# Kernel tuning notes

Hardware: AMD Instinct MI355X
Metric: run time of the kernel (lower is better)

## Reference

```python
import jax, jax.numpy as jnp
import numpy as np

B, L, D, H = 8, 512, 1024, 16
HD = D // H
DIST_VOCAB = 64
NEG = -1e9


def setup_inputs() -> dict:
    key = jax.random.key(0)
    ks = jax.random.split(key, 16)
    inp = {}
    inp['q'] = jax.random.normal(ks[0], (B, L, D), jnp.float32)
    inp['k'] = jax.random.normal(ks[1], (B, L, D), jnp.float32)
    inp['v'] = jax.random.normal(ks[2], (B, L, D), jnp.float32)
    s = 1.0 / np.sqrt(D)
    inp['Wq'] = jax.random.normal(ks[3], (D, D), jnp.float32) * s
    inp['bq'] = jnp.zeros((D,), jnp.float32)
    inp['Wk'] = jax.random.normal(ks[4], (D, D), jnp.float32) * s
    inp['bk'] = jnp.zeros((D,), jnp.float32)
    inp['Wv'] = jax.random.normal(ks[5], (D, D), jnp.float32) * s
    inp['bv'] = jnp.zeros((D,), jnp.float32)
    inp['Wo'] = jax.random.normal(ks[6], (D, D), jnp.float32) * s
    inp['bo'] = jnp.zeros((D,), jnp.float32)
    inp['dist_emb'] = jax.random.normal(ks[7], (DIST_VOCAB, H), jnp.float32) * (1.0 / np.sqrt(H))
    # sinusoidal positional table (1, L, D), rank-3 as asserted in AttentionBase
    pos = np.arange(L)[:, None]
    dim = np.arange(D)[None, :]
    ang = pos / np.power(10000.0, (2 * (dim // 2)) / D)
    pe = np.where(dim % 2 == 0, np.sin(ang), np.cos(ang)).astype(np.float32)
    inp['sin_enc'] = jnp.asarray(pe)[None]
    inp['length'] = jax.random.randint(ks[8], (B,), L // 2, L + 1, jnp.int32)
    inp['dist'] = jax.random.randint(ks[9], (B, L, L), 0, DIST_VOCAB, jnp.int32)
    return inp


def _rope(x, sin_pos, cos_pos):
    # x: (B, L, D). rotate-half interleaved: [-x1, x0, -x3, x2, ...]
    x_shift = jnp.stack([-x[..., 1::2], x[..., 0::2]], axis=-1).reshape(x.shape)
    return x * cos_pos + x_shift * sin_pos


def reference(q, k, v, Wq, bq, Wk, bk, Wv, bv, Wo, bo, dist_emb, sin_enc, length, dist):
    # linear projections (torch Linear: x @ W.T + b)
    qp = q @ Wq.T + bq
    kp = k @ Wk.T + bk
    vp = v @ Wv.T + bv
    # rope (pe='rope', cls_len=0, step=0)
    sin_pos = jnp.repeat(sin_enc[:, :L, 0::2], 2, axis=-1)
    cos_pos = jnp.repeat(sin_enc[:, :L, 1::2], 2, axis=-1)
    qp = _rope(qp, sin_pos, cos_pos)
    kp = _rope(kp, sin_pos, cos_pos)
    # split heads -> (B, H, L, HD)
    qh = qp.reshape(B, L, H, HD).transpose(0, 2, 1, 3)
    kh = kp.reshape(B, L, H, HD).transpose(0, 2, 1, 3)
    vh = vp.reshape(B, L, H, HD).transpose(0, 2, 1, 3)
    # scale (scale_length=0 -> 1/sqrt(d_head))
    qh = qh * (1.0 / np.sqrt(HD))
    scores = jnp.einsum('bhqd,bhkd->bhqk', qh, kh)
    # relative 'dist' bias: (B,L,L,H) -> (B,H,L,L)
    scores = scores + dist_emb[dist].transpose(0, 3, 1, 2)
    # padding mask: key positions >= valid length (future=False)
    key_mask = jnp.arange(L)[None, :] >= length[:, None]  # (B, L)
    scores = jnp.where(key_mask[:, None, None, :], NEG, scores)
    attn = jax.nn.softmax(scores, axis=-1)  # dropout p=0.0 => identity
    out = jnp.einsum('bhqk,bhkd->bhqd', attn, vh)
    out = out.transpose(0, 2, 1, 3).reshape(B, L, D)
    return out @ Wo.T + bo
```

## Files before the change

kernel.cpp:

```cpp
#include <hip/hip_runtime.h>
#include <stdint.h>

typedef unsigned short u16;
typedef __bf16 bf16x8 __attribute__((ext_vector_type(8)));
typedef float f32x4 __attribute__((ext_vector_type(4)));

#define MFMA16(a, b, c) __builtin_amdgcn_mfma_f32_16x16x32_bf16(a, b, c, 0, 0, 0)

__device__ __forceinline__ float b2f(u16 u) { return __uint_as_float(((uint32_t)u) << 16); }
__device__ __forceinline__ u16 f2b(float f) {
    uint32_t x = __float_as_uint(f);
    return (u16)((x + 0x7fffu + ((x >> 16) & 1u)) >> 16);
}
__device__ __forceinline__ void load16(const void* g, void* l) {
    __builtin_amdgcn_global_load_lds(
        (const __attribute__((address_space(1))) uint32_t*)(uintptr_t)g,
        (__attribute__((address_space(3))) uint32_t*)(uint32_t)(uintptr_t)l,
        16, 0, 0);
}
__device__ __forceinline__ bf16x8 ld8f(const float* f) {
    float4 a = *(const float4*)f;
    float4 b = *(const float4*)(f + 4);
    bf16x8 o;
    o[0] = (__bf16)a.x; o[1] = (__bf16)a.y; o[2] = (__bf16)a.z; o[3] = (__bf16)a.w;
    o[4] = (__bf16)b.x; o[5] = (__bf16)b.y; o[6] = (__bf16)b.z; o[7] = (__bf16)b.w;
    return o;
}

__global__ __launch_bounds__(256) void convert_k(
    const float* __restrict__ q, const float* __restrict__ k, const float* __restrict__ v,
    const float* __restrict__ Wq, const float* __restrict__ Wk,
    const float* __restrict__ Wv, const float* __restrict__ Wo,
    u16* __restrict__ qb, u16* __restrict__ kb, u16* __restrict__ vb,
    u16* __restrict__ wqb, u16* __restrict__ wkb, u16* __restrict__ wvb,
    u16* __restrict__ wob)
{
    const float* src; u16* dst; int n8;
    switch (blockIdx.y) {
        case 0: src = q;  dst = qb;  n8 = 524288; break;
        case 1: src = k;  dst = kb;  n8 = 524288; break;
        case 2: src = v;  dst = vb;  n8 = 524288; break;
        case 3: src = Wq; dst = wqb; n8 = 131072; break;
        case 4: src = Wk; dst = wkb; n8 = 131072; break;
        case 5: src = Wv; dst = wvb; n8 = 131072; break;
        default: src = Wo; dst = wob; n8 = 131072; break;
    }
    int i = blockIdx.x * 256 + threadIdx.x;
    if (i >= n8) return;
    bf16x8 o = ld8f(src + (size_t)i * 8);
    *(bf16x8*)(dst + (size_t)i * 8) = o;
}

__global__ __launch_bounds__(256) void gemm_proj_b(
    const u16* __restrict__ qb, const u16* __restrict__ kb, const u16* __restrict__ vb,
    const u16* __restrict__ wqb, const u16* __restrict__ wkb, const u16* __restrict__ wvb,
    const float* __restrict__ bq, const float* __restrict__ bk, const float* __restrict__ bv,
    const float* __restrict__ sin_enc,
    u16* __restrict__ qh, u16* __restrict__ kh, u16* __restrict__ vt)
{
    __shared__ __align__(16) u16 lA[128 * 32];
    __shared__ __align__(16) u16 lB[128 * 32];
    const int t = threadIdx.x, wave = t >> 6, lane = t & 63;
    const int bx = blockIdx.x;
    const int w_idx = bx >> 3;
    const int n0 = (bx & 7) << 7;
    const int m0 = blockIdx.y << 7;
    const u16* A = (w_idx == 0) ? qb : (w_idx == 1 ? kb : vb);
    const u16* W = (w_idx == 0) ? wqb : (w_idx == 1 ? wkb : wvb);
    const float* bias = (w_idx == 0) ? bq : (w_idx == 1 ? bk : bv);

    const int wr = wave >> 1, wc = wave & 1;
    const int col16 = lane & 15, g16 = lane >> 4;
    f32x4 acc[4][4] = {};

    const int r0  = wave * 32 + (lane >> 2);
    const int kc8 = (lane & 3) << 3;
    const u16* gA = A + (size_t)(m0 + r0) * 1024 + kc8;
    const u16* gB = W + (size_t)(n0 + r0) * 1024 + kc8;
    char* lA0 = (char*)lA + wave * 2048;
    char* lB0 = (char*)lB + wave * 2048;

    for (int kk = 0; kk < 1024; kk += 32) {
        load16(gA + kk, lA0);
        load16(gA + kk + 16 * 1024, lA0 + 1024);
        load16(gB + kk, lB0);
        load16(gB + kk + 16 * 1024, lB0 + 1024);
        __syncthreads();
        const u16* pA = lA + (wr * 64 + col16) * 32 + g16 * 8;
        const u16* pB = lB + (wc * 64 + col16) * 32 + g16 * 8;
        bf16x8 af[4], bfr[4];
#pragma unroll
        for (int i = 0; i < 4; i++) {
            af[i]  = *(const bf16x8*)(pA + i * 512);
            bfr[i] = *(const bf16x8*)(pB + i * 512);
        }
#pragma unroll
        for (int mi = 0; mi < 4; mi++)
#pragma unroll
            for (int ni = 0; ni < 4; ni++)
                acc[mi][ni] = MFMA16(af[mi], bfr[ni], acc[mi][ni]);
        __syncthreads();
    }

#pragma unroll
    for (int ni = 0; ni < 4; ni++) {
        const int n = n0 + wc * 64 + ni * 16 + col16;
        const float bn = bias[n];
        const int h = n >> 6, hd = n & 63;
#pragma unroll
        for (int mi = 0; mi < 4; mi++) {
#pragma unroll
            for (int r = 0; r < 4; r++) {
                const int m = m0 + wr * 64 + mi * 16 + g16 * 4 + r;
                const int b = m >> 9, l = m & 511;
                float x = acc[mi][ni][r] + bn;
                if (w_idx == 2) {
                    vt[((size_t)(b * 16 + h) * 64 + hd) * 512 + l] = f2b(x);
                } else {
                    float partner = __shfl_xor(x, 1);
                    float s = sin_enc[(size_t)l * 1024 + (n & ~1)];
                    float c = sin_enc[(size_t)l * 1024 + (n | 1)];
                    float y = (n & 1) ? (x * c + partner * s) : (x * c - partner * s);
                    if (w_idx == 0) y *= 0.125f;
                    u16* dst = (w_idx == 0) ? qh : kh;
                    dst[((size_t)(b * 16 + h) * 512 + l) * 64 + hd] = f2b(y);
                }
            }
        }
    }
}

__global__ __launch_bounds__(256) void gemm_proj_f32(
    const float* __restrict__ qin, const float* __restrict__ kin, const float* __restrict__ vin,
    const float* __restrict__ Wq, const float* __restrict__ bq,
    const float* __restrict__ Wk, const float* __restrict__ bk,
    const float* __restrict__ Wv, const float* __restrict__ bv,
    const float* __restrict__ sin_enc,
    u16* __restrict__ qh, u16* __restrict__ kh, u16* __restrict__ vt)
{
    __shared__ __align__(16) u16 lA[128 * 32];
    __shared__ __align__(16) u16 lB[128 * 32];
    const int t = threadIdx.x, wave = t >> 6, lane = t & 63;
    const int bx = blockIdx.x;
    const int w_idx = bx >> 3;
    const int n0 = (bx & 7) << 7;
    const int m0 = blockIdx.y << 7;
    const float* A    = (w_idx == 0) ? qin : (w_idx == 1 ? kin : vin);
    const float* W    = (w_idx == 0) ? Wq  : (w_idx == 1 ? Wk  : Wv);
    const float* bias = (w_idx == 0) ? bq  : (w_idx == 1 ? bk  : bv);

    const int wr = wave >> 1, wc = wave & 1;
    const int col16 = lane & 15, g16 = lane >> 4;
    f32x4 acc[4][4] = {};

    const int c0   = wave * 128 + lane;
    const int row0 = c0 >> 2;
    const int kp   = (c0 & 3) << 3;
    const size_t gA0 = (size_t)(m0 + row0) * 1024 + kp;
    const size_t gB0 = (size_t)(n0 + row0) * 1024 + kp;
    u16* wA0 = lA + c0 * 8;
    u16* wA1 = lA + (c0 + 64) * 8;
    u16* wB0 = lB + c0 * 8;
    u16* wB1 = lB + (c0 + 64) * 8;

    bf16x8 ra0 = ld8f(A + gA0);
    bf16x8 ra1 = ld8f(A + gA0 + 16 * 1024);
    bf16x8 rb0 = ld8f(W + gB0);
    bf16x8 rb1 = ld8f(W + gB0 + 16 * 1024);

    for (int kk = 32; kk <= 1024; kk += 32) {
        __syncthreads();
        *(bf16x8*)wA0 = ra0; *(bf16x8*)wA1 = ra1;
        *(bf16x8*)wB0 = rb0; *(bf16x8*)wB1 = rb1;
        __syncthreads();
        if (kk < 1024) {
            ra0 = ld8f(A + gA0 + kk);
            ra1 = ld8f(A + gA0 + kk + 16 * 1024);
            rb0 = ld8f(W + gB0 + kk);
            rb1 = ld8f(W + gB0 + kk + 16 * 1024);
        }
        const u16* pA = lA + (wr * 64 + col16) * 32 + g16 * 8;
        const u16* pB = lB + (wc * 64 + col16) * 32 + g16 * 8;
        bf16x8 af[4], bfr[4];
#pragma unroll
        for (int i = 0; i < 4; i++) {
            af[i]  = *(const bf16x8*)(pA + i * 512);
            bfr[i] = *(const bf16x8*)(pB + i * 512);
        }
#pragma unroll
        for (int mi = 0; mi < 4; mi++)
#pragma unroll
            for (int ni = 0; ni < 4; ni++)
                acc[mi][ni] = MFMA16(af[mi], bfr[ni], acc[mi][ni]);
    }

#pragma unroll
    for (int ni = 0; ni < 4; ni++) {
        const int n = n0 + wc * 64 + ni * 16 + col16;
        const float bn = bias[n];
        const int h = n >> 6, hd = n & 63;
#pragma unroll
        for (int mi = 0; mi < 4; mi++) {
#pragma unroll
            for (int r = 0; r < 4; r++) {
                const int m = m0 + wr * 64 + mi * 16 + g16 * 4 + r;
                const int b = m >> 9, l = m & 511;
                float x = acc[mi][ni][r] + bn;
                if (w_idx == 2) {
                    vt[((size_t)(b * 16 + h) * 64 + hd) * 512 + l] = f2b(x);
                } else {
                    float partner = __shfl_xor(x, 1);
                    float s = sin_enc[(size_t)l * 1024 + (n & ~1)];
                    float c = sin_enc[(size_t)l * 1024 + (n | 1)];
                    float y = (n & 1) ? (x * c + partner * s) : (x * c - partner * s);
                    if (w_idx == 0) y *= 0.125f;
                    u16* dst = (w_idx == 0) ? qh : kh;
                    dst[((size_t)(b * 16 + h) * 512 + l) * 64 + hd] = f2b(y);
                }
            }
        }
    }
}

__global__ __launch_bounds__(256) void attn_kernel(
    const u16* __restrict__ qh, const u16* __restrict__ kh, const u16* __restrict__ vt,
    const float* __restrict__ demb_g, const int* __restrict__ length,
    const int* __restrict__ dist, u16* __restrict__ ctx)
{
    __shared__ __align__(16) u16 Qs[64 * 64];
    __shared__ __align__(16) u16 Ks[64 * 64];
    __shared__ __align__(16) u16 Vs[64 * 64];
    __shared__ __align__(16) u16 Ps[4][16 * 64];
    __shared__ float demb[64];

    const int t = threadIdx.x, wave = t >> 6, lane = t & 63;
    const int bxx = blockIdx.x;
    const int qt = bxx & 7, bh = bxx >> 3;
    const int b = bh >> 4, h = bh & 15;
    if (t < 64) demb[t] = demb_g[t * 16 + h];
    const int len_b = length[b];
    const int ktmax = (len_b + 63) >> 6;
    const int col16 = lane & 15, g16 = lane >> 4;
    const int c0 = wave * 128 + lane, c1 = c0 + 64;

    const u16* qbase = qh + (size_t)(bh * 512 + qt * 64) * 64;
    {
        uint4 rq0 = *(const uint4*)(qbase + c0 * 8);
        uint4 rq1 = *(const uint4*)(qbase + c1 * 8);
        *(uint4*)((char*)Qs + c0 * 16) = rq0;
        *(uint4*)((char*)Qs + c1 * 16) = rq1;
    }

    const u16* kbase = kh + (size_t)bh * 512 * 64;
    const u16* vbase = vt + (size_t)bh * 64 * 512;
    const int* dist_b = dist + (size_t)b * 512 * 512;
    const int qrow_base = qt * 64 + wave * 16 + g16 * 4;

    uint4 rk0 = *(const uint4*)(kbase + c0 * 8);
    uint4 rk1 = *(const uint4*)(kbase + c1 * 8);
    uint4 rv0 = *(const uint4*)(vbase + (size_t)(c0 >> 3) * 512 + (c0 & 7) * 8);
    uint4 rv1 = *(const uint4*)(vbase + (size_t)(c1 >> 3) * 512 + (c1 & 7) * 8);

    __syncthreads();
    const u16* pQ = Qs + (wave * 16 + col16) * 64 + g16 * 8;
    const bf16x8 qa0 = *(const bf16x8*)pQ;
    const bf16x8 qa1 = *(const bf16x8*)(pQ + 32);

    f32x4 oacc[4] = {};
    float mrow[4], lrow[4];
#pragma unroll
    for (int r = 0; r < 4; r++) { mrow[r] = -1e30f; lrow[r] = 0.f; }

    for (int kt = 0; kt < ktmax; kt++) {
        __syncthreads();
        *(uint4*)((char*)Ks + c0 * 16) = rk0;
        *(uint4*)((char*)Ks + c1 * 16) = rk1;
        *(uint4*)((char*)Vs + c0 * 16) = rv0;
        *(uint4*)((char*)Vs + c1 * 16) = rv1;
        __syncthreads();
        if (kt + 1 < ktmax) {
            const u16* kb = kbase + (size_t)(kt + 1) * 64 * 64;
            rk0 = *(const uint4*)(kb + c0 * 8);
            rk1 = *(const uint4*)(kb + c1 * 8);
            rv0 = *(const uint4*)(vbase + (size_t)(c0 >> 3) * 512 + (kt + 1) * 64 + (c0 & 7) * 8);
            rv1 = *(const uint4*)(vbase + (size_t)(c1 >> 3) * 512 + (kt + 1) * 64 + (c1 & 7) * 8);
        }

        f32x4 sacc[4] = {};
#pragma unroll
        for (int ni = 0; ni < 4; ni++) {
            const u16* pK = Ks + (ni * 16 + col16) * 64 + g16 * 8;
            bf16x8 kf0 = *(const bf16x8*)pK;
            bf16x8 kf1 = *(const bf16x8*)(pK + 32);
            sacc[ni] = MFMA16(qa0, kf0, sacc[ni]);
            sacc[ni] = MFMA16(qa1, kf1, sacc[ni]);
        }

        float rmax[4] = {-1e30f, -1e30f, -1e30f, -1e30f};
#pragma unroll
        for (int ni = 0; ni < 4; ni++) {
            const int kcol = kt * 64 + ni * 16 + col16;
            const bool masked = kcol >= len_b;
#pragma unroll
            for (int r = 0; r < 4; r++) {
                const int qrow = qrow_base + r;
                float s = sacc[ni][r] + demb[dist_b[(size_t)qrow * 512 + kcol] & 63];
                s = masked ? -1e9f : s;
                sacc[ni][r] = s;
                rmax[r] = fmaxf(rmax[r], s);
            }
        }
#pragma unroll
        for (int off = 1; off < 16; off <<= 1)
#pragma unroll
            for (int r = 0; r < 4; r++) rmax[r] = fmaxf(rmax[r], __shfl_xor(rmax[r], off));

        float alpha[4], rsum[4];
#pragma unroll
        for (int r = 0; r < 4; r++) {
            float mn = fmaxf(mrow[r], rmax[r]);
            alpha[r] = __expf(mrow[r] - mn);
            mrow[r] = mn;
            rsum[r] = 0.f;
        }
#pragma unroll
        for (int ni = 0; ni < 4; ni++)
#pragma unroll
            for (int r = 0; r < 4; r++) {
                float p = __expf(sacc[ni][r] - mrow[r]);
                sacc[ni][r] = p;
                rsum[r] += p;
            }
#pragma unroll
        for (int off = 1; off < 16; off <<= 1)
#pragma unroll
            for (int r = 0; r < 4; r++) rsum[r] += __shfl_xor(rsum[r], off);
#pragma unroll
        for (int r = 0; r < 4; r++) lrow[r] = lrow[r] * alpha[r] + rsum[r];
#pragma unroll
        for (int di = 0; di < 4; di++)
#pragma unroll
            for (int r = 0; r < 4; r++) oacc[di][r] *= alpha[r];

        u16* Pw = &Ps[wave][0];
#pragma unroll
        for (int ni = 0; ni < 4; ni++)
#pragma unroll
            for (int r = 0; r < 4; r++)
                Pw[(g16 * 4 + r) * 64 + ni * 16 + col16] = f2b(sacc[ni][r]);
        __syncthreads();

        const u16* pP = Pw + col16 * 64 + g16 * 8;
        bf16x8 pa0 = *(const bf16x8*)pP;
        bf16x8 pa1 = *(const bf16x8*)(pP + 32);
#pragma unroll
        for (int di = 0; di < 4; di++) {
            const u16* pV = Vs + (di * 16 + col16) * 64 + g16 * 8;
            bf16x8 vf0 = *(const bf16x8*)pV;
            bf16x8 vf1 = *(const bf16x8*)(pV + 32);
            oacc[di] = MFMA16(pa0, vf0, oacc[di]);
            oacc[di] = MFMA16(pa1, vf1, oacc[di]);
        }
    }

#pragma unroll
    for (int di = 0; di < 4; di++)
#pragma unroll
        for (int r = 0; r < 4; r++) {
            const int qrow = qrow_base + r;
            const int d = di * 16 + col16;
            const float inv_l = 1.0f / fmaxf(lrow[r], 1e-30f);
            ctx[(size_t)(b * 512 + qrow) * 1024 + h * 64 + d] = f2b(oacc[di][r] * inv_l);
        }
}

__global__ __launch_bounds__(256) void gemm_out_b(
    const u16* __restrict__ ctx, const u16* __restrict__ wob,
    const float* __restrict__ bo, float* __restrict__ out)
{
    __shared__ __align__(16) u16 lA[128 * 32];
    __shared__ __align__(16) u16 lB[128 * 32];
    const int t = threadIdx.x, wave = t >> 6, lane = t & 63;
    const int n0 = blockIdx.x << 7;
    const int m0 = blockIdx.y << 7;
    const int wr = wave >> 1, wc = wave & 1;
    const int col16 = lane & 15, g16 = lane >> 4;
    f32x4 acc[4][4] = {};

    const int r0  = wave * 32 + (lane >> 2);
    const int kc8 = (lane & 3) << 3;
    const u16* gA = ctx + (size_t)(m0 + r0) * 1024 + kc8;
    const u16* gB = wob + (size_t)(n0 + r0) * 1024 + kc8;
    char* lA0 = (char*)lA + wave * 2048;
    char* lB0 = (char*)lB + wave * 2048;

    for (int kk = 0; kk < 1024; kk += 32) {
        load16(gA + kk, lA0);
        load16(gA + kk + 16 * 1024, lA0 + 1024);
        load16(gB + kk, lB0);
        load16(gB + kk + 16 * 1024, lB0 + 1024);
        __syncthreads();
        const u16* pA = lA + (wr * 64 + col16) * 32 + g16 * 8;
        const u16* pB = lB + (wc * 64 + col16) * 32 + g16 * 8;
        bf16x8 af[4], bfr[4];
#pragma unroll
        for (int i = 0; i < 4; i++) {
            af[i]  = *(const bf16x8*)(pA + i * 512);
            bfr[i] = *(const bf16x8*)(pB + i * 512);
        }
#pragma unroll
        for (int mi = 0; mi < 4; mi++)
#pragma unroll
            for (int ni = 0; ni < 4; ni++)
                acc[mi][ni] = MFMA16(af[mi], bfr[ni], acc[mi][ni]);
        __syncthreads();
    }

#pragma unroll
    for (int ni = 0; ni < 4; ni++) {
        const int n = n0 + wc * 64 + ni * 16 + col16;
        const float bn = bo[n];
#pragma unroll
        for (int mi = 0; mi < 4; mi++)
#pragma unroll
            for (int r = 0; r < 4; r++) {
                const int m = m0 + wr * 64 + mi * 16 + g16 * 4 + r;
                out[(size_t)m * 1024 + n] = acc[mi][ni][r] + bn;
            }
    }
}

__global__ __launch_bounds__(256) void gemm_out_f32(
    const u16* __restrict__ ctx, const float* __restrict__ Wo,
    const float* __restrict__ bo, float* __restrict__ out)
{
    __shared__ __align__(16) u16 lA[128 * 32];
    __shared__ __align__(16) u16 lB[128 * 32];
    const int t = threadIdx.x, wave = t >> 6, lane = t & 63;
    const int n0 = blockIdx.x << 7;
    const int m0 = blockIdx.y << 7;
    const int wr = wave >> 1, wc = wave & 1;
    const int col16 = lane & 15, g16 = lane >> 4;
    f32x4 acc[4][4] = {};

    const int c0   = wave * 128 + lane;
    const int row0 = c0 >> 2;
    const int kp   = (c0 & 3) << 3;
    const u16* gA = ctx + (size_t)(m0 + row0) * 1024 + kp;
    const size_t gB0 = (size_t)(n0 + row0) * 1024 + kp;
    u16* wA0 = lA + c0 * 8;
    u16* wA1 = lA + (c0 + 64) * 8;
    u16* wB0 = lB + c0 * 8;
    u16* wB1 = lB + (c0 + 64) * 8;

    uint4 ua0 = *(const uint4*)gA;
    uint4 ua1 = *(const uint4*)(gA + 16 * 1024);
    bf16x8 ra0 = *(bf16x8*)&ua0, ra1 = *(bf16x8*)&ua1;
    bf16x8 rb0 = ld8f(Wo + gB0);
    bf16x8 rb1 = ld8f(Wo + gB0 + 16 * 1024);

    for (int kk = 32; kk <= 1024; kk += 32) {
        __syncthreads();
        *(bf16x8*)wA0 = ra0; *(bf16x8*)wA1 = ra1;
        *(bf16x8*)wB0 = rb0; *(bf16x8*)wB1 = rb1;
        __syncthreads();
        if (kk < 1024) {
            uint4 t0 = *(const uint4*)(gA + kk);
            uint4 t1 = *(const uint4*)(gA + kk + 16 * 1024);
            ra0 = *(bf16x8*)&t0; ra1 = *(bf16x8*)&t1;
            rb0 = ld8f(Wo + gB0 + kk);
            rb1 = ld8f(Wo + gB0 + kk + 16 * 1024);
        }
        const u16* pA = lA + (wr * 64 + col16) * 32 + g16 * 8;
        const u16* pB = lB + (wc * 64 + col16) * 32 + g16 * 8;
        bf16x8 af[4], bfr[4];
#pragma unroll
        for (int i = 0; i < 4; i++) {
            af[i]  = *(const bf16x8*)(pA + i * 512);
            bfr[i] = *(const bf16x8*)(pB + i * 512);
        }
#pragma unroll
        for (int mi = 0; mi < 4; mi++)
#pragma unroll
            for (int ni = 0; ni < 4; ni++)
                acc[mi][ni] = MFMA16(af[mi], bfr[ni], acc[mi][ni]);
    }

#pragma unroll
    for (int ni = 0; ni < 4; ni++) {
        const int n = n0 + wc * 64 + ni * 16 + col16;
        const float bn = bo[n];
#pragma unroll
        for (int mi = 0; mi < 4; mi++)
#pragma unroll
            for (int r = 0; r < 4; r++) {
                const int m = m0 + wr * 64 + mi * 16 + g16 * 4 + r;
                out[(size_t)m * 1024 + n] = acc[mi][ni][r] + bn;
            }
    }
}

extern "C" void kernel_launch(void* const* d_in, const int* in_sizes, int n_in,
                              void* d_out, int out_size, void* d_ws, size_t ws_size,
                              hipStream_t stream) {
    const float* q       = (const float*)d_in[0];
    const float* k       = (const float*)d_in[1];
    const float* v       = (const float*)d_in[2];
    const float* Wq      = (const float*)d_in[3];
    const float* bq      = (const float*)d_in[4];
    const float* Wk      = (const float*)d_in[5];
    const float* bk      = (const float*)d_in[6];
    const float* Wv      = (const float*)d_in[7];
    const float* bv      = (const float*)d_in[8];
    const float* Wo      = (const float*)d_in[9];
    const float* bo      = (const float*)d_in[10];
    const float* demb    = (const float*)d_in[11];
    const float* sin_enc = (const float*)d_in[12];
    const int* length    = (const int*)d_in[13];
    const int* dist      = (const int*)d_in[14];

    const size_t SLOT = 4194304;
    u16* qh  = (u16*)d_ws;
    u16* kh  = qh + SLOT;
    u16* vt  = kh + SLOT;
    u16* ctx = vt + SLOT;

    if (ws_size >= (size_t)64 * 1024 * 1024) {
        u16* qb  = ctx + SLOT;
        u16* kb  = qb + SLOT;
        u16* vb  = kb + SLOT;
        u16* wqb = vb + SLOT;
        u16* wkb = wqb + 1048576;
        u16* wvb = wkb + 1048576;
        u16* wob = wvb + 1048576;
        convert_k<<<dim3(2048, 7), 256, 0, stream>>>(q, k, v, Wq, Wk, Wv, Wo,
                                                     qb, kb, vb, wqb, wkb, wvb, wob);
        gemm_proj_b<<<dim3(24, 32), 256, 0, stream>>>(qb, kb, vb, wqb, wkb, wvb,
                                                      bq, bk, bv, sin_enc, qh, kh, vt);
        attn_kernel<<<dim3(1024), 256, 0, stream>>>(qh, kh, vt, demb, length, dist, ctx);
        gemm_out_b<<<dim3(8, 32), 256, 0, stream>>>(ctx, wob, bo, (float*)d_out);
    } else {
        gemm_proj_f32<<<dim3(24, 32), 256, 0, stream>>>(q, k, v, Wq, bq, Wk, bk, Wv, bv,
                                                        sin_enc, qh, kh, vt);
        attn_kernel<<<dim3(1024), 256, 0, stream>>>(qh, kh, vt, demb, length, dist, ctx);
        gemm_out_f32<<<dim3(8, 32), 256, 0, stream>>>(ctx, Wo, bo, (float*)d_out);
    }
}
```

Baseline: 287.4 us.

## Double-buffer GEMM LDS tiles, stage dist bias in LDS, shrink output GEMM tile

The projection and output GEMMs now use double-buffered LDS tiles, so the async global-to-LDS load of the next K slice overlaps the MFMAs on the current one. The output GEMM also drops to 64x128 tiles with twice as many blocks, which gives better CU occupancy on a small grid. In the attention kernel, each dist tile is prefetched with coalesced vector loads into registers, packed into bytes in LDS, and read from there, replacing scattered per-element global loads. These changes cost more LDS per block and extra register pressure.

```diff
diff --git a/kernel.cpp b/kernel.cpp
--- a/kernel.cpp
+++ b/kernel.cpp
@@ -58,8 +58,8 @@
     const float* __restrict__ sin_enc,
     u16* __restrict__ qh, u16* __restrict__ kh, u16* __restrict__ vt)
 {
-    __shared__ __align__(16) u16 lA[128 * 32];
-    __shared__ __align__(16) u16 lB[128 * 32];
+    __shared__ __align__(16) u16 lA[2][128 * 32];
+    __shared__ __align__(16) u16 lB[2][128 * 32];
     const int t = threadIdx.x, wave = t >> 6, lane = t & 63;
     const int bx = blockIdx.x;
     const int w_idx = bx >> 3;
@@ -77,30 +77,45 @@
     const int kc8 = (lane & 3) << 3;
     const u16* gA = A + (size_t)(m0 + r0) * 1024 + kc8;
     const u16* gB = W + (size_t)(n0 + r0) * 1024 + kc8;
-    char* lA0 = (char*)lA + wave * 2048;
-    char* lB0 = (char*)lB + wave * 2048;
-
-    for (int kk = 0; kk < 1024; kk += 32) {
-        load16(gA + kk, lA0);
-        load16(gA + kk + 16 * 1024, lA0 + 1024);
-        load16(gB + kk, lB0);
-        load16(gB + kk + 16 * 1024, lB0 + 1024);
-        __syncthreads();
-        const u16* pA = lA + (wr * 64 + col16) * 32 + g16 * 8;
-        const u16* pB = lB + (wc * 64 + col16) * 32 + g16 * 8;
-        bf16x8 af[4], bfr[4];
-#pragma unroll
-        for (int i = 0; i < 4; i++) {
-            af[i]  = *(const bf16x8*)(pA + i * 512);
-            bfr[i] = *(const bf16x8*)(pB + i * 512);
-        }
-#pragma unroll
-        for (int mi = 0; mi < 4; mi++)
-#pragma unroll
-            for (int ni = 0; ni < 4; ni++)
-                acc[mi][ni] = MFMA16(af[mi], bfr[ni], acc[mi][ni]);
-        __syncthreads();
-    }
+
+#define PROJ_STAGE(kk, buf)                                             \
+    do {                                                                \
+        char* a0 = (char*)lA[buf] + wave * 2048;                        \
+        char* b0 = (char*)lB[buf] + wave * 2048;                        \
+        load16(gA + (kk), a0);                                          \
+        load16(gA + (kk) + 16 * 1024, a0 + 1024);                       \
+        load16(gB + (kk), b0);                                          \
+        load16(gB + (kk) + 16 * 1024, b0 + 1024);                       \
+    } while (0)
+
+#define PROJ_COMPUTE(buf)                                               \
+    do {                                                                \
+        const u16* pA = lA[buf] + (wr * 64 + col16) * 32 + g16 * 8;     \
+        const u16* pB = lB[buf] + (wc * 64 + col16) * 32 + g16 * 8;     \
+        bf16x8 af[4], bfr[4];                                           \
+        _Pragma("unroll")                                               \
+        for (int i = 0; i < 4; i++) {                                   \
+            af[i]  = *(const bf16x8*)(pA + i * 512);                    \
+            bfr[i] = *(const bf16x8*)(pB + i * 512);                    \
+        }                                                               \
+        _Pragma("unroll")                                               \
+        for (int mi = 0; mi < 4; mi++)                                  \
+            _Pragma("unroll")                                           \
+            for (int ni = 0; ni < 4; ni++)                              \
+                acc[mi][ni] = MFMA16(af[mi], bfr[ni], acc[mi][ni]);     \
+    } while (0)
+
+    PROJ_STAGE(0, 0);
+    for (int kk = 0; kk < 1024; kk += 64) {
+        __syncthreads();
+        if (kk + 32 < 1024) PROJ_STAGE(kk + 32, 1);
+        PROJ_COMPUTE(0);
+        __syncthreads();
+        if (kk + 64 < 1024) PROJ_STAGE(kk + 64, 0);
+        PROJ_COMPUTE(1);
+    }
+#undef PROJ_STAGE
+#undef PROJ_COMPUTE
 
 #pragma unroll
     for (int ni = 0; ni < 4; ni++) {
@@ -231,6 +246,7 @@
     __shared__ __align__(16) u16 Ks[64 * 64];
     __shared__ __align__(16) u16 Vs[64 * 64];
     __shared__ __align__(16) u16 Ps[4][16 * 64];
+    __shared__ __align__(16) uint8_t Ds[64 * 64];
     __shared__ float demb[64];
 
     const int t = threadIdx.x, wave = t >> 6, lane = t & 63;
@@ -253,13 +269,20 @@
 
     const u16* kbase = kh + (size_t)bh * 512 * 64;
     const u16* vbase = vt + (size_t)bh * 64 * 512;
-    const int* dist_b = dist + (size_t)b * 512 * 512;
     const int qrow_base = qt * 64 + wave * 16 + g16 * 4;
+
+    const int drow = t >> 2;
+    const int dcol = (t & 3) << 4;
+    const int* dg = dist + (size_t)b * 512 * 512 + (size_t)(qt * 64 + drow) * 512 + dcol;
+    uint32_t* DsW = (uint32_t*)(Ds + drow * 64 + dcol);
 
     uint4 rk0 = *(const uint4*)(kbase + c0 * 8);
     uint4 rk1 = *(const uint4*)(kbase + c1 * 8);
     uint4 rv0 = *(const uint4*)(vbase + (size_t)(c0 >> 3) * 512 + (c0 & 7) * 8);
     uint4 rv1 = *(const uint4*)(vbase + (size_t)(c1 >> 3) * 512 + (c1 & 7) * 8);
+    int4 dd[4];
+#pragma unroll
+    for (int j = 0; j < 4; j++) dd[j] = *(const int4*)(dg + j * 4);
 
     __syncthreads();
     const u16* pQ = Qs + (wave * 16 + col16) * 64 + g16 * 8;
@@ -277,6 +300,10 @@
         *(uint4*)((char*)Ks + c1 * 16) = rk1;
         *(uint4*)((char*)Vs + c0 * 16) = rv0;
         *(uint4*)((char*)Vs + c1 * 16) = rv1;
+#pragma unroll
+        for (int j = 0; j < 4; j++)
+            DsW[j] = (uint32_t)(dd[j].x & 63) | ((uint32_t)(dd[j].y & 63) << 8) |
+                     ((uint32_t)(dd[j].z & 63) << 16) | ((uint32_t)(dd[j].w & 63) << 24);
         __syncthreads();
         if (kt + 1 < ktmax) {
             const u16* kb = kbase + (size_t)(kt + 1) * 64 * 64;
@@ -284,6 +311,9 @@
             rk1 = *(const uint4*)(kb + c1 * 8);
             rv0 = *(const uint4*)(vbase + (size_t)(c0 >> 3) * 512 + (kt + 1) * 64 + (c0 & 7) * 8);
             rv1 = *(const uint4*)(vbase + (size_t)(c1 >> 3) * 512 + (kt + 1) * 64 + (c1 & 7) * 8);
+            const int* dgn = dg + (kt + 1) * 64;
+#pragma unroll
+            for (int j = 0; j < 4; j++) dd[j] = *(const int4*)(dgn + j * 4);
         }
 
         f32x4 sacc[4] = {};
@@ -297,14 +327,14 @@
         }
 
         float rmax[4] = {-1e30f, -1e30f, -1e30f, -1e30f};
+        const int qrl = wave * 16 + g16 * 4;
 #pragma unroll
         for (int ni = 0; ni < 4; ni++) {
-            const int kcol = kt * 64 + ni * 16 + col16;
-            const bool masked = kcol >= len_b;
+            const int kcl = ni * 16 + col16;
+            const bool masked = (kt * 64 + kcl) >= len_b;
 #pragma unroll
             for (int r = 0; r < 4; r++) {
-                const int qrow = qrow_base + r;
-                float s = sacc[ni][r] + demb[dist_b[(size_t)qrow * 512 + kcol] & 63];
+                float s = sacc[ni][r] + demb[Ds[(qrl + r) * 64 + kcl]];
                 s = masked ? -1e9f : s;
                 sacc[ni][r] = s;
                 rmax[r] = fmaxf(rmax[r], s);
@@ -378,53 +408,65 @@
     const u16* __restrict__ ctx, const u16* __restrict__ wob,
     const float* __restrict__ bo, float* __restrict__ out)
 {
-    __shared__ __align__(16) u16 lA[128 * 32];
-    __shared__ __align__(16) u16 lB[128 * 32];
+    __shared__ __align__(16) u16 lA[2][64 * 32];
+    __shared__ __align__(16) u16 lB[2][128 * 32];
     const int t = threadIdx.x, wave = t >> 6, lane = t & 63;
     const int n0 = blockIdx.x << 7;
-    const int m0 = blockIdx.y << 7;
-    const int wr = wave >> 1, wc = wave & 1;
+    const int m0 = blockIdx.y << 6;
     const int col16 = lane & 15, g16 = lane >> 4;
-    f32x4 acc[4][4] = {};
-
-    const int r0  = wave * 32 + (lane >> 2);
-    const int kc8 = (lane & 3) << 3;
-    const u16* gA = ctx + (size_t)(m0 + r0) * 1024 + kc8;
-    const u16* gB = wob + (size_t)(n0 + r0) * 1024 + kc8;
-    char* lA0 = (char*)lA + wave * 2048;
-    char* lB0 = (char*)lB + wave * 2048;
-
-    for (int kk = 0; kk < 1024; kk += 32) {
-        load16(gA + kk, lA0);
-        load16(gA + kk + 16 * 1024, lA0 + 1024);
-        load16(gB + kk, lB0);
-        load16(gB + kk + 16 * 1024, lB0 + 1024);
-        __syncthreads();
-        const u16* pA = lA + (wr * 64 + col16) * 32 + g16 * 8;
-        const u16* pB = lB + (wc * 64 + col16) * 32 + g16 * 8;
-        bf16x8 af[4], bfr[4];
-#pragma unroll
-        for (int i = 0; i < 4; i++) {
-            af[i]  = *(const bf16x8*)(pA + i * 512);
-            bfr[i] = *(const bf16x8*)(pB + i * 512);
-        }
+    f32x4 acc[4][2] = {};
+
+    const int cA = wave * 64 + lane;
+    const u16* gA = ctx + (size_t)(m0 + (cA >> 2)) * 1024 + ((cA & 3) << 3);
+    const int cB = wave * 128 + lane;
+    const u16* gB = wob + (size_t)(n0 + (cB >> 2)) * 1024 + ((cB & 3) << 3);
+
+#define OUT_STAGE(kk, buf)                                              \
+    do {                                                                \
+        char* a0 = (char*)lA[buf] + wave * 1024;                        \
+        char* b0 = (char*)lB[buf] + wave * 2048;                        \
+        load16(gA + (kk), a0);                                          \
+        load16(gB + (kk), b0);                                          \
+        load16(gB + (kk) + 16 * 1024, b0 + 1024);                       \
+    } while (0)
+
+#define OUT_COMPUTE(buf)                                                \
+    do {                                                                \
+        const u16* pA = lA[buf] + col16 * 32 + g16 * 8;                 \
+        const u16* pB = lB[buf] + (wave * 32 + col16) * 32 + g16 * 8;   \
+        bf16x8 af[4], bfr[2];                                           \
+        _Pragma("unroll")                                               \
+        for (int i = 0; i < 4; i++) af[i] = *(const bf16x8*)(pA + i * 512); \
+        _Pragma("unroll")                                               \
+        for (int i = 0; i < 2; i++) bfr[i] = *(const bf16x8*)(pB + i * 512); \
+        _Pragma("unroll")                                               \
+        for (int mi = 0; mi < 4; mi++)                                  \
+            _Pragma("unroll")                                           \
+            for (int ni = 0; ni < 2; ni++)                              \
+                acc[mi][ni] = MFMA16(af[mi], bfr[ni], acc[mi][ni]);     \
+    } while (0)
+
+    OUT_STAGE(0, 0);
+    for (int kk = 0; kk < 1024; kk += 64) {
+        __syncthreads();
+        if (kk + 32 < 1024) OUT_STAGE(kk + 32, 1);
+        OUT_COMPUTE(0);
+        __syncthreads();
+        if (kk + 64 < 1024) OUT_STAGE(kk + 64, 0);
+        OUT_COMPUTE(1);
+    }
+#undef OUT_STAGE
+#undef OUT_COMPUTE
+
+#pragma unroll
+    for (int ni = 0; ni < 2; ni++) {
+        const int n = n0 + wave * 32 + ni * 16 + col16;
+        const float bn = bo[n];
 #pragma unroll
         for (int mi = 0; mi < 4; mi++)
 #pragma unroll
-            for (int ni = 0; ni < 4; ni++)
-                acc[mi][ni] = MFMA16(af[mi], bfr[ni], acc[mi][ni]);
-        __syncthreads();
-    }
-
-#pragma unroll
-    for (int ni = 0; ni < 4; ni++) {
-        const int n = n0 + wc * 64 + ni * 16 + col16;
-        const float bn = bo[n];
-#pragma unroll
-        for (int mi = 0; mi < 4; mi++)
-#pragma unroll
             for (int r = 0; r < 4; r++) {
-                const int m = m0 + wr * 64 + mi * 16 + g16 * 4 + r;
+                const int m = m0 + mi * 16 + g16 * 4 + r;
                 out[(size_t)m * 1024 + n] = acc[mi][ni][r] + bn;
             }
     }
@@ -538,7 +580,7 @@
         gemm_proj_b<<<dim3(24, 32), 256, 0, stream>>>(qb, kb, vb, wqb, wkb, wvb,
                                                       bq, bk, bv, sin_enc, qh, kh, vt);
         attn_kernel<<<dim3(1024), 256, 0, stream>>>(qh, kh, vt, demb, length, dist, ctx);
-        gemm_out_b<<<dim3(8, 32), 256, 0, stream>>>(ctx, wob, bo, (float*)d_out);
+        gemm_out_b<<<dim3(8, 64), 256, 0, stream>>>(ctx, wob, bo, (float*)d_out);
     } else {
         gemm_proj_f32<<<dim3(24, 32), 256, 0, stream>>>(q, k, v, Wq, bq, Wk, bk, Wv, bv,
                                                         sin_enc, qh, kh, vt);
```

After: 270.8 us. 1.06x faster.

## Fuse activation conversion into projection GEMM, double-buffer GEMMs, stage dist in LDS

Applied to the files above, without the earlier changes.

The projection GEMM now reads fp32 activations directly and converts them to bf16 while staging into LDS, so the separate conversion pass over q/k/v and its round trip through workspace are removed. Both the projection and output GEMMs use smaller tiles with double-buffered LDS, which drops one barrier per k-step and launches more blocks. The attention kernel prefetches each dist tile into registers, packs the indices into bytes in LDS, and reads the bias from there instead of doing scattered global gathers. In exchange, smaller tiles reuse each loaded operand less, and the in-loop conversion adds VALU work to the GEMM.

```diff
diff --git a/kernel.cpp b/kernel.cpp
--- a/kernel.cpp
+++ b/kernel.cpp
@@ -26,80 +26,92 @@
     o[4] = (__bf16)b.x; o[5] = (__bf16)b.y; o[6] = (__bf16)b.z; o[7] = (__bf16)b.w;
     return o;
 }
+__device__ __forceinline__ bf16x8 cvt8(float4 a, float4 b) {
+    bf16x8 o;
+    o[0] = (__bf16)a.x; o[1] = (__bf16)a.y; o[2] = (__bf16)a.z; o[3] = (__bf16)a.w;
+    o[4] = (__bf16)b.x; o[5] = (__bf16)b.y; o[6] = (__bf16)b.z; o[7] = (__bf16)b.w;
+    return o;
+}
 
 __global__ __launch_bounds__(256) void convert_k(
-    const float* __restrict__ q, const float* __restrict__ k, const float* __restrict__ v,
     const float* __restrict__ Wq, const float* __restrict__ Wk,
     const float* __restrict__ Wv, const float* __restrict__ Wo,
-    u16* __restrict__ qb, u16* __restrict__ kb, u16* __restrict__ vb,
     u16* __restrict__ wqb, u16* __restrict__ wkb, u16* __restrict__ wvb,
     u16* __restrict__ wob)
 {
-    const float* src; u16* dst; int n8;
+    const float* src; u16* dst;
     switch (blockIdx.y) {
-        case 0: src = q;  dst = qb;  n8 = 524288; break;
-        case 1: src = k;  dst = kb;  n8 = 524288; break;
-        case 2: src = v;  dst = vb;  n8 = 524288; break;
-        case 3: src = Wq; dst = wqb; n8 = 131072; break;
-        case 4: src = Wk; dst = wkb; n8 = 131072; break;
-        case 5: src = Wv; dst = wvb; n8 = 131072; break;
-        default: src = Wo; dst = wob; n8 = 131072; break;
+        case 0:  src = Wq; dst = wqb; break;
+        case 1:  src = Wk; dst = wkb; break;
+        case 2:  src = Wv; dst = wvb; break;
+        default: src = Wo; dst = wob; break;
     }
     int i = blockIdx.x * 256 + threadIdx.x;
-    if (i >= n8) return;
     bf16x8 o = ld8f(src + (size_t)i * 8);
     *(bf16x8*)(dst + (size_t)i * 8) = o;
 }
 
-__global__ __launch_bounds__(256) void gemm_proj_b(
-    const u16* __restrict__ qb, const u16* __restrict__ kb, const u16* __restrict__ vb,
+__global__ __launch_bounds__(256, 5) void gemm_proj_b(
+    const float* __restrict__ qf, const float* __restrict__ kf, const float* __restrict__ vf,
     const u16* __restrict__ wqb, const u16* __restrict__ wkb, const u16* __restrict__ wvb,
     const float* __restrict__ bq, const float* __restrict__ bk, const float* __restrict__ bv,
     const float* __restrict__ sin_enc,
     u16* __restrict__ qh, u16* __restrict__ kh, u16* __restrict__ vt)
 {
-    __shared__ __align__(16) u16 lA[128 * 32];
-    __shared__ __align__(16) u16 lB[128 * 32];
+    __shared__ __align__(16) u16 lA[2][64 * 32];
+    __shared__ __align__(16) u16 lB[2][128 * 32];
     const int t = threadIdx.x, wave = t >> 6, lane = t & 63;
     const int bx = blockIdx.x;
     const int w_idx = bx >> 3;
     const int n0 = (bx & 7) << 7;
-    const int m0 = blockIdx.y << 7;
-    const u16* A = (w_idx == 0) ? qb : (w_idx == 1 ? kb : vb);
-    const u16* W = (w_idx == 0) ? wqb : (w_idx == 1 ? wkb : wvb);
+    const int m0 = blockIdx.y << 6;
+    const float* A = (w_idx == 0) ? qf : (w_idx == 1 ? kf : vf);
+    const u16*   W = (w_idx == 0) ? wqb : (w_idx == 1 ? wkb : wvb);
     const float* bias = (w_idx == 0) ? bq : (w_idx == 1 ? bk : bv);
 
     const int wr = wave >> 1, wc = wave & 1;
     const int col16 = lane & 15, g16 = lane >> 4;
-    f32x4 acc[4][4] = {};
-
-    const int r0  = wave * 32 + (lane >> 2);
-    const int kc8 = (lane & 3) << 3;
-    const u16* gA = A + (size_t)(m0 + r0) * 1024 + kc8;
-    const u16* gB = W + (size_t)(n0 + r0) * 1024 + kc8;
-    char* lA0 = (char*)lA + wave * 2048;
-    char* lB0 = (char*)lB + wave * 2048;
-
-    for (int kk = 0; kk < 1024; kk += 32) {
-        load16(gA + kk, lA0);
-        load16(gA + kk + 16 * 1024, lA0 + 1024);
-        load16(gB + kk, lB0);
-        load16(gB + kk + 16 * 1024, lB0 + 1024);
-        __syncthreads();
-        const u16* pA = lA + (wr * 64 + col16) * 32 + g16 * 8;
-        const u16* pB = lB + (wc * 64 + col16) * 32 + g16 * 8;
-        bf16x8 af[4], bfr[4];
-#pragma unroll
-        for (int i = 0; i < 4; i++) {
-            af[i]  = *(const bf16x8*)(pA + i * 512);
-            bfr[i] = *(const bf16x8*)(pB + i * 512);
-        }
-#pragma unroll
-        for (int mi = 0; mi < 4; mi++)
+    f32x4 acc[2][4] = {};
+
+    const float* gA = A + (size_t)(m0 + (t >> 2)) * 1024 + ((t & 3) << 3);
+    u16* wA0 = lA[0] + t * 8;
+    u16* wA1 = lA[1] + t * 8;
+    const int c0 = wave * 128 + lane;
+    const u16* gB = W + (size_t)(n0 + (c0 >> 2)) * 1024 + ((c0 & 3) << 3);
+
+    float4 ra0 = *(const float4*)(gA);
+    float4 ra1 = *(const float4*)(gA + 4);
+    load16(gB, (char*)lB[0] + wave * 2048);
+    load16(gB + 16 * 1024, (char*)lB[0] + wave * 2048 + 1024);
+    *(bf16x8*)wA0 = cvt8(ra0, ra1);
+    ra0 = *(const float4*)(gA + 32);
+    ra1 = *(const float4*)(gA + 36);
+
+    for (int it = 0; it < 32; ++it) {
+        const int buf = it & 1, nbuf = buf ^ 1;
+        __syncthreads();
+        if (it + 1 < 32) {
+            *(bf16x8*)(nbuf ? wA1 : wA0) = cvt8(ra0, ra1);
+            const int kk = (it + 1) << 5;
+            load16(gB + kk, (char*)lB[nbuf] + wave * 2048);
+            load16(gB + kk + 16 * 1024, (char*)lB[nbuf] + wave * 2048 + 1024);
+            if (it + 2 < 32) {
+                ra0 = *(const float4*)(gA + (it + 2) * 32);
+                ra1 = *(const float4*)(gA + (it + 2) * 32 + 4);
+            }
+        }
+        const u16* pA = lA[buf] + (wr * 32 + col16) * 32 + g16 * 8;
+        const u16* pB = lB[buf] + (wc * 64 + col16) * 32 + g16 * 8;
+        bf16x8 af[2], bfr[4];
+#pragma unroll
+        for (int i = 0; i < 2; i++) af[i] = *(const bf16x8*)(pA + i * 512);
+#pragma unroll
+        for (int i = 0; i < 4; i++) bfr[i] = *(const bf16x8*)(pB + i * 512);
+#pragma unroll
+        for (int mi = 0; mi < 2; mi++)
 #pragma unroll
             for (int ni = 0; ni < 4; ni++)
                 acc[mi][ni] = MFMA16(af[mi], bfr[ni], acc[mi][ni]);
-        __syncthreads();
     }
 
 #pragma unroll
@@ -108,10 +120,10 @@
         const float bn = bias[n];
         const int h = n >> 6, hd = n & 63;
 #pragma unroll
-        for (int mi = 0; mi < 4; mi++) {
+        for (int mi = 0; mi < 2; mi++) {
 #pragma unroll
             for (int r = 0; r < 4; r++) {
-                const int m = m0 + wr * 64 + mi * 16 + g16 * 4 + r;
+                const int m = m0 + wr * 32 + mi * 16 + g16 * 4 + r;
                 const int b = m >> 9, l = m & 511;
                 float x = acc[mi][ni][r] + bn;
                 if (w_idx == 2) {
@@ -231,6 +243,7 @@
     __shared__ __align__(16) u16 Ks[64 * 64];
     __shared__ __align__(16) u16 Vs[64 * 64];
     __shared__ __align__(16) u16 Ps[4][16 * 64];
+    __shared__ __align__(16) uint8_t Ds[64 * 64];
     __shared__ float demb[64];
 
     const int t = threadIdx.x, wave = t >> 6, lane = t & 63;
@@ -253,13 +266,20 @@
 
     const u16* kbase = kh + (size_t)bh * 512 * 64;
     const u16* vbase = vt + (size_t)bh * 64 * 512;
-    const int* dist_b = dist + (size_t)b * 512 * 512;
     const int qrow_base = qt * 64 + wave * 16 + g16 * 4;
+
+    const int drow = t >> 2;
+    const int dcol = (t & 3) << 4;
+    const int* dg = dist + (size_t)b * 512 * 512 + (size_t)(qt * 64 + drow) * 512 + dcol;
+    uint32_t* DsW = (uint32_t*)(Ds + drow * 64 + dcol);
 
     uint4 rk0 = *(const uint4*)(kbase + c0 * 8);
     uint4 rk1 = *(const uint4*)(kbase + c1 * 8);
     uint4 rv0 = *(const uint4*)(vbase + (size_t)(c0 >> 3) * 512 + (c0 & 7) * 8);
     uint4 rv1 = *(const uint4*)(vbase + (size_t)(c1 >> 3) * 512 + (c1 & 7) * 8);
+    int4 dd[4];
+#pragma unroll
+    for (int j = 0; j < 4; j++) dd[j] = *(const int4*)(dg + j * 4);
 
     __syncthreads();
     const u16* pQ = Qs + (wave * 16 + col16) * 64 + g16 * 8;
@@ -277,6 +297,10 @@
         *(uint4*)((char*)Ks + c1 * 16) = rk1;
         *(uint4*)((char*)Vs + c0 * 16) = rv0;
         *(uint4*)((char*)Vs + c1 * 16) = rv1;
+#pragma unroll
+        for (int j = 0; j < 4; j++)
+            DsW[j] = (uint32_t)(dd[j].x & 63) | ((uint32_t)(dd[j].y & 63) << 8) |
+                     ((uint32_t)(dd[j].z & 63) << 16) | ((uint32_t)(dd[j].w & 63) << 24);
         __syncthreads();
         if (kt + 1 < ktmax) {
             const u16* kb = kbase + (size_t)(kt + 1) * 64 * 64;
@@ -284,6 +308,9 @@
             rk1 = *(const uint4*)(kb + c1 * 8);
             rv0 = *(const uint4*)(vbase + (size_t)(c0 >> 3) * 512 + (kt + 1) * 64 + (c0 & 7) * 8);
             rv1 = *(const uint4*)(vbase + (size_t)(c1 >> 3) * 512 + (kt + 1) * 64 + (c1 & 7) * 8);
+            const int* dgn = dg + (kt + 1) * 64;
+#pragma unroll
+            for (int j = 0; j < 4; j++) dd[j] = *(const int4*)(dgn + j * 4);
         }
 
         f32x4 sacc[4] = {};
@@ -297,14 +324,14 @@
         }
 
         float rmax[4] = {-1e30f, -1e30f, -1e30f, -1e30f};
+        const int qrl = wave * 16 + g16 * 4;
 #pragma unroll
         for (int ni = 0; ni < 4; ni++) {
-            const int kcol = kt * 64 + ni * 16 + col16;
-            const bool masked = kcol >= len_b;
+            const int kcl = ni * 16 + col16;
+            const bool masked = (kt * 64 + kcl) >= len_b;
 #pragma unroll
             for (int r = 0; r < 4; r++) {
-                const int qrow = qrow_base + r;
-                float s = sacc[ni][r] + demb[dist_b[(size_t)qrow * 512 + kcol] & 63];
+                float s = sacc[ni][r] + demb[Ds[(qrl + r) * 64 + kcl]];
                 s = masked ? -1e9f : s;
                 sacc[ni][r] = s;
                 rmax[r] = fmaxf(rmax[r], s);
@@ -374,57 +401,58 @@
         }
 }
 
-__global__ __launch_bounds__(256) void gemm_out_b(
+__global__ __launch_bounds__(256, 4) void gemm_out_b(
     const u16* __restrict__ ctx, const u16* __restrict__ wob,
     const float* __restrict__ bo, float* __restrict__ out)
 {
-    __shared__ __align__(16) u16 lA[128 * 32];
-    __shared__ __align__(16) u16 lB[128 * 32];
+    __shared__ __align__(16) u16 lA[2][64 * 32];
+    __shared__ __align__(16) u16 lB[2][64 * 32];
     const int t = threadIdx.x, wave = t >> 6, lane = t & 63;
-    const int n0 = blockIdx.x << 7;
-    const int m0 = blockIdx.y << 7;
+    const int n0 = blockIdx.x << 6;
+    const int m0 = blockIdx.y << 6;
     const int wr = wave >> 1, wc = wave & 1;
     const int col16 = lane & 15, g16 = lane >> 4;
-    f32x4 acc[4][4] = {};
-
-    const int r0  = wave * 32 + (lane >> 2);
-    const int kc8 = (lane & 3) << 3;
-    const u16* gA = ctx + (size_t)(m0 + r0) * 1024 + kc8;
-    const u16* gB = wob + (size_t)(n0 + r0) * 1024 + kc8;
-    char* lA0 = (char*)lA + wave * 2048;
-    char* lB0 = (char*)lB + wave * 2048;
-
-    for (int kk = 0; kk < 1024; kk += 32) {
-        load16(gA + kk, lA0);
-        load16(gA + kk + 16 * 1024, lA0 + 1024);
-        load16(gB + kk, lB0);
-        load16(gB + kk + 16 * 1024, lB0 + 1024);
-        __syncthreads();
-        const u16* pA = lA + (wr * 64 + col16) * 32 + g16 * 8;
-        const u16* pB = lB + (wc * 64 + col16) * 32 + g16 * 8;
-        bf16x8 af[4], bfr[4];
-#pragma unroll
-        for (int i = 0; i < 4; i++) {
+    f32x4 acc[2][2] = {};
+
+    const int cA = wave * 64 + lane;
+    const u16* gA = ctx + (size_t)(m0 + (cA >> 2)) * 1024 + ((cA & 3) << 3);
+    const u16* gB = wob + (size_t)(n0 + (cA >> 2)) * 1024 + ((cA & 3) << 3);
+
+    load16(gA, (char*)lA[0] + wave * 1024);
+    load16(gB, (char*)lB[0] + wave * 1024);
+
+    for (int it = 0; it < 32; ++it) {
+        const int buf = it & 1, nbuf = buf ^ 1;
+        __syncthreads();
+        if (it + 1 < 32) {
+            const int kk = (it + 1) << 5;
+            load16(gA + kk, (char*)lA[nbuf] + wave * 1024);
+            load16(gB + kk, (char*)lB[nbuf] + wave * 1024);
+        }
+        const u16* pA = lA[buf] + (wr * 32 + col16) * 32 + g16 * 8;
+        const u16* pB = lB[buf] + (wc * 32 + col16) * 32 + g16 * 8;
+        bf16x8 af[2], bfr[2];
+#pragma unroll
+        for (int i = 0; i < 2; i++) {
             af[i]  = *(const bf16x8*)(pA + i * 512);
             bfr[i] = *(const bf16x8*)(pB + i * 512);
         }
 #pragma unroll
-        for (int mi = 0; mi < 4; mi++)
-#pragma unroll
-            for (int ni = 0; ni < 4; ni++)
+        for (int mi = 0; mi < 2; mi++)
+#pragma unroll
+            for (int ni = 0; ni < 2; ni++)
                 acc[mi][ni] = MFMA16(af[mi], bfr[ni], acc[mi][ni]);
-        __syncthreads();
-    }
-
-#pragma unroll
-    for (int ni = 0; ni < 4; ni++) {
-        const int n = n0 + wc * 64 + ni * 16 + col16;
+    }
+
+#pragma unroll
+    for (int ni = 0; ni < 2; ni++) {
+        const int n = n0 + wc * 32 + ni * 16 + col16;
         const float bn = bo[n];
 #pragma unroll
-        for (int mi = 0; mi < 4; mi++)
+        for (int mi = 0; mi < 2; mi++)
 #pragma unroll
             for (int r = 0; r < 4; r++) {
-                const int m = m0 + wr * 64 + mi * 16 + g16 * 4 + r;
+                const int m = m0 + wr * 32 + mi * 16 + g16 * 4 + r;
                 out[(size_t)m * 1024 + n] = acc[mi][ni][r] + bn;
             }
     }
@@ -526,19 +554,15 @@
     u16* ctx = vt + SLOT;
 
     if (ws_size >= (size_t)64 * 1024 * 1024) {
-        u16* qb  = ctx + SLOT;
-        u16* kb  = qb + SLOT;
-        u16* vb  = kb + SLOT;
-        u16* wqb = vb + SLOT;
+        u16* wqb = ctx + SLOT;
         u16* wkb = wqb + 1048576;
         u16* wvb = wkb + 1048576;
         u16* wob = wvb + 1048576;
-        convert_k<<<dim3(2048, 7), 256, 0, stream>>>(q, k, v, Wq, Wk, Wv, Wo,
-                                                     qb, kb, vb, wqb, wkb, wvb, wob);
-        gemm_proj_b<<<dim3(24, 32), 256, 0, stream>>>(qb, kb, vb, wqb, wkb, wvb,
+        convert_k<<<dim3(512, 4), 256, 0, stream>>>(Wq, Wk, Wv, Wo, wqb, wkb, wvb, wob);
+        gemm_proj_b<<<dim3(24, 64), 256, 0, stream>>>(q, k, v, wqb, wkb, wvb,
                                                       bq, bk, bv, sin_enc, qh, kh, vt);
         attn_kernel<<<dim3(1024), 256, 0, stream>>>(qh, kh, vt, demb, length, dist, ctx);
-        gemm_out_b<<<dim3(8, 32), 256, 0, stream>>>(ctx, wob, bo, (float*)d_out);
+        gemm_out_b<<<dim3(16, 64), 256, 0, stream>>>(ctx, wob, bo, (float*)d_out);
     } else {
         gemm_proj_f32<<<dim3(24, 32), 256, 0, stream>>>(q, k, v, Wq, bq, Wk, bk, Wv, bv,
                                                         sin_enc, qh, kh, vt);
```

After: 274.4 us. 1.05x faster.
